# Kernel tuning notes

Measured on AMD Instinct MI355X. Metric: run time of the kernel, lower is better.

Reference implementation:

```python
import jax, jax.numpy as jnp
import numpy as np

N_EMBD = 768
N_HEAD = 12
HEAD_SIZE = N_EMBD // N_HEAD  # 64
WINDOW = 64  # sliding_window_size
EPS = 1e-6


def _rmsnorm(x, g):
    xf = x.astype(jnp.float32)
    n = xf * jax.lax.rsqrt(jnp.mean(xf * xf, axis=-1, keepdims=True) + EPS)
    return n.astype(x.dtype) * g


def _gelu_tanh(x):
    c = jnp.sqrt(jnp.asarray(2.0 / jnp.pi, x.dtype))
    return 0.5 * x * (1.0 + jnp.tanh(c * (x + 0.044715 * x ** 3)))


def setup_inputs() -> dict:
    key = jax.random.key(0)
    ks = jax.random.split(key, 12)
    B, T = 8, 1024
    s = 0.02
    return {
        "x": jax.random.normal(ks[0], (B, T, N_EMBD), jnp.float32),
        "w_q": jax.random.normal(ks[1], (N_EMBD, N_HEAD, HEAD_SIZE), jnp.float32) * s,
        "w_k": jax.random.normal(ks[2], (N_EMBD, N_HEAD, HEAD_SIZE), jnp.float32) * s,
        "w_v": jax.random.normal(ks[3], (N_EMBD, N_HEAD, HEAD_SIZE), jnp.float32) * s,
        "w_proj": jax.random.normal(ks[4], (N_EMBD, N_EMBD), jnp.float32) * s,
        "b_proj": jnp.zeros((N_EMBD,), jnp.float32),
        "w_ff1": jax.random.normal(ks[5], (N_EMBD, 4 * N_EMBD), jnp.float32) * s,
        "b_ff1": jnp.zeros((4 * N_EMBD,), jnp.float32),
        "w_ff2": jax.random.normal(ks[6], (4 * N_EMBD, N_EMBD), jnp.float32) * s,
        "b_ff2": jnp.zeros((N_EMBD,), jnp.float32),
        "g1": jnp.ones((N_EMBD,), jnp.float32),
        "g2": jnp.ones((N_EMBD,), jnp.float32),
    }


def reference(x, w_q, w_k, w_v, w_proj, b_proj, w_ff1, b_ff1, w_ff2, b_ff2, g1, g2):
    B, T, C = x.shape
    # ---- multi-head sliding-window causal attention (eval: dropout = identity) ----
    h = _rmsnorm(x, g1)
    q = jnp.einsum("btc,chd->bhtd", h, w_q)
    k = jnp.einsum("btc,chd->bhtd", h, w_k)
    v = jnp.einsum("btc,chd->bhtd", h, w_v)
    scores = jnp.einsum("bhtd,bhsd->bhts", q, k) / jnp.sqrt(jnp.asarray(HEAD_SIZE, x.dtype))
    pos = jnp.arange(T)
    diff = pos[:, None] - pos[None, :]  # q_pos - k_pos
    mask = (diff < 0) | (diff >= WINDOW)  # causal + sliding window of 64
    scores = jnp.where(mask[None, None], jnp.asarray(-jnp.inf, scores.dtype), scores)
    attn = jax.nn.softmax(scores, axis=-1)
    out = jnp.einsum("bhts,bhsd->bhtd", attn, v)
    out = out.transpose(0, 2, 1, 3).reshape(B, T, C)  # concat heads
    x = x + out @ w_proj + b_proj
    # ---- feedforward ----
    h2 = _rmsnorm(x, g2)
    ff = _gelu_tanh(h2 @ w_ff1 + b_ff1) @ w_ff2 + b_ff2
    x = x + ff
    aux = jnp.asarray(0.0, jnp.float32)
    return (x, aux)
```

## Files before the change

### kernel.cpp

```cpp
#include <hip/hip_runtime.h>
#include <cstdint>

#define DEVI __device__ __forceinline__

typedef __bf16 bf16x8 __attribute__((ext_vector_type(8)));
typedef float  f32x4  __attribute__((ext_vector_type(4)));

template<int V> struct IC { static constexpr int v = V; };

DEVI unsigned short f2b(float f){
  unsigned u = __builtin_bit_cast(unsigned, f);
  unsigned r = u + 0x7FFF + ((u >> 16) & 1);
  return (unsigned short)(r >> 16);
}
DEVI float b2f(unsigned short s){
  unsigned u = ((unsigned)s) << 16;
  return __builtin_bit_cast(float, u);
}
DEVI float gelu_f(float x){
  float u = 0.7978845608028654f * (x + 0.044715f * x * x * x);
  float e = __expf(2.0f * u);
  return x * (1.0f - 1.0f / (e + 1.0f));
}
DEVI void gl_lds16(const unsigned short* g, unsigned short* l){
  __builtin_amdgcn_global_load_lds(
      (const __attribute__((address_space(1))) unsigned int*)g,
      (__attribute__((address_space(3))) unsigned int*)l, 16, 0, 0);
}

__global__ __launch_bounds__(256)
void transpose_all(const float* __restrict__ w_q, const float* __restrict__ w_k,
                   const float* __restrict__ w_v, const float* __restrict__ w_proj,
                   const float* __restrict__ w_ff1, const float* __restrict__ w_ff2,
                   unsigned short* __restrict__ WqkvT, unsigned short* __restrict__ WprojT,
                   unsigned short* __restrict__ Wff1T, unsigned short* __restrict__ Wff2T)
{
  __shared__ float tile[32][33];
  int blk = blockIdx.x;
  const float* in; unsigned short* out; int R, C, b0;
  if      (blk < 576) { in = w_q;    out = WqkvT;              R = 768;  C = 768;  b0 = 0;    }
  else if (blk < 1152){ in = w_k;    out = WqkvT + 768 * 768;  R = 768;  C = 768;  b0 = 576;  }
  else if (blk < 1728){ in = w_v;    out = WqkvT + 1536 * 768; R = 768;  C = 768;  b0 = 1152; }
  else if (blk < 2304){ in = w_proj; out = WprojT;             R = 768;  C = 768;  b0 = 1728; }
  else if (blk < 4608){ in = w_ff1;  out = Wff1T;              R = 768;  C = 3072; b0 = 2304; }
  else                { in = w_ff2;  out = Wff2T;              R = 3072; C = 768;  b0 = 4608; }
  int lb = blk - b0;
  int nbx = C >> 5;
  int bx = lb % nbx, by = lb / nbx;
  int c0 = bx << 5, r0 = by << 5;
  int tx = threadIdx.x & 31, ty = threadIdx.x >> 5;
  #pragma unroll
  for (int j = 0; j < 32; j += 8)
    tile[ty + j][tx] = in[(size_t)(r0 + ty + j) * C + c0 + tx];
  __syncthreads();
  #pragma unroll
  for (int j = 0; j < 32; j += 8)
    out[(size_t)(c0 + ty + j) * R + r0 + tx] = f2b(tile[tx][ty + j]);
}

__global__ __launch_bounds__(256)
void rmsnorm_k(const float* __restrict__ x, const float* __restrict__ g,
               unsigned short* __restrict__ out)
{
  int wid = threadIdx.x >> 6, lane = threadIdx.x & 63;
  size_t row = (size_t)blockIdx.x * 4 + wid;
  const float* xr = x + row * 768;
  float4 v[3];
  float ss = 0.0f;
  #pragma unroll
  for (int c = 0; c < 3; c++){
    v[c] = *(const float4*)&xr[lane * 4 + c * 256];
    ss += v[c].x * v[c].x + v[c].y * v[c].y + v[c].z * v[c].z + v[c].w * v[c].w;
  }
  #pragma unroll
  for (int o = 32; o >= 1; o >>= 1) ss += __shfl_xor(ss, o);
  float rs = rsqrtf(ss * (1.0f / 768.0f) + 1e-6f);
  #pragma unroll
  for (int c = 0; c < 3; c++){
    const float4 gv = *(const float4*)&g[lane * 4 + c * 256];
    ushort4 o4;
    o4.x = f2b(v[c].x * rs * gv.x);
    o4.y = f2b(v[c].y * rs * gv.y);
    o4.z = f2b(v[c].z * rs * gv.z);
    o4.w = f2b(v[c].w * rs * gv.w);
    *(ushort4*)&out[row * 768 + lane * 4 + c * 256] = o4;
  }
}

template<bool BIAS, bool GELU_, bool RES, bool OUTF32>
__global__ __launch_bounds__(256, 3)
void gemm_db(const unsigned short* __restrict__ A, const unsigned short* __restrict__ Bt,
             const float* __restrict__ bias, const float* __restrict__ res,
             void* __restrict__ outp, int M, int N, int K)
{
  constexpr int BM = 64;
  constexpr int MI = 2;
  constexpr int AL = 2;
  constexpr int BUFSZ = (BM + 128) * 64;
  __shared__ unsigned short sm[2][BUFSZ];

  int tid = threadIdx.x, wid = tid >> 6, lane = tid & 63;
  int la = lane & 15, hi = lane >> 4;
  int wm = wid >> 1, wn = wid & 1;
  int tiles_n = N >> 7;
  int bid = blockIdx.x;
  bid = (bid & 7) * (gridDim.x >> 3) + (bid >> 3);
  int m0 = (bid / tiles_n) * BM, n0 = (bid % tiles_n) << 7;
  int NT = K >> 6;

  f32x4 acc[MI][4] = {};

  const unsigned short* aSrc[AL];
  const unsigned short* bSrc[4];
  unsigned short* aDst[2][AL];
  unsigned short* bDst[2][4];
  #pragma unroll
  for (int l = 0; l < AL; l++){
    int cb = wid * (BM * 2) + l * 64;
    int idx = cb + lane;
    int row = idx >> 3, sl2 = (idx & 7) ^ (row & 7);
    aSrc[l] = A + (size_t)(m0 + row) * K + sl2 * 8;
    aDst[0][l] = &sm[0][cb * 8];
    aDst[1][l] = &sm[1][cb * 8];
  }
  #pragma unroll
  for (int l = 0; l < 4; l++){
    int cb = wid * 256 + l * 64;
    int idx = cb + lane;
    int row = idx >> 3, sl2 = (idx & 7) ^ (row & 7);
    bSrc[l] = Bt + (size_t)(n0 + row) * K + sl2 * 8;
    bDst[0][l] = &sm[0][BM * 64 + cb * 8];
    bDst[1][l] = &sm[1][BM * 64 + cb * 8];
  }

  const unsigned short* fa[2][2];
  const unsigned short* fb[2][2];
  #pragma unroll
  for (int bf = 0; bf < 2; bf++)
    #pragma unroll
    for (int kk = 0; kk < 2; kk++){
      int sw = (((kk * 4 + hi) ^ (la & 7))) * 8;
      fa[bf][kk] = &sm[bf][(wm * (BM / 2) + la) * 64 + sw];
      fb[bf][kk] = &sm[bf][BM * 64 + (wn * 64 + la) * 64 + sw];
    }

  auto stageTo = [&](auto BF){
    constexpr int bf = decltype(BF)::v;
    #pragma unroll
    for (int l = 0; l < AL; l++){ gl_lds16(aSrc[l], aDst[bf][l]); aSrc[l] += 64; }
    #pragma unroll
    for (int l = 0; l < 4; l++){ gl_lds16(bSrc[l], bDst[bf][l]); bSrc[l] += 64; }
  };

  stageTo(IC<0>{});

  auto tile_step = [&](auto BUF, int t){
    constexpr int CB = decltype(BUF)::v;
    if (t + 1 < NT){
      stageTo(IC<CB ^ 1>{});
      asm volatile("s_waitcnt vmcnt(6)" ::: "memory");
    } else {
      asm volatile("s_waitcnt vmcnt(0)" ::: "memory");
    }
    __builtin_amdgcn_s_barrier();

    bf16x8 afr[MI][2], bfr[4][2];
    #pragma unroll
    for (int mm = 0; mm < MI; mm++){
      afr[mm][0] = *(const bf16x8*)(fa[CB][0] + mm * 1024);
      afr[mm][1] = *(const bf16x8*)(fa[CB][1] + mm * 1024);
    }
    #pragma unroll
    for (int nn = 0; nn < 4; nn++){
      bfr[nn][0] = *(const bf16x8*)(fb[CB][0] + nn * 1024);
      bfr[nn][1] = *(const bf16x8*)(fb[CB][1] + nn * 1024);
    }
    __builtin_amdgcn_s_setprio(1);
    #pragma unroll
    for (int mm = 0; mm < MI; mm++)
      #pragma unroll
      for (int nn = 0; nn < 4; nn++)
        #pragma unroll
        for (int kk = 0; kk < 2; kk++)
          acc[mm][nn] = __builtin_amdgcn_mfma_f32_16x16x32_bf16(
              afr[mm][kk], bfr[nn][kk], acc[mm][nn], 0, 0, 0);
    __builtin_amdgcn_s_setprio(0);

    __builtin_amdgcn_s_barrier();
  };

  for (int t = 0; t < NT; t += 2){
    tile_step(IC<0>{}, t);
    tile_step(IC<1>{}, t + 1);
  }

  float* outF = (float*)outp;
  unsigned short* outB = (unsigned short*)outp;
  #pragma unroll
  for (int mm = 0; mm < MI; mm++){
    int rowb = m0 + wm * (BM / 2) + mm * 16 + hi * 4;
    #pragma unroll
    for (int nn = 0; nn < 4; nn++){
      int col = n0 + wn * 64 + nn * 16 + la;
      float bv = BIAS ? bias[col] : 0.0f;
      #pragma unroll
      for (int r = 0; r < 4; r++){
        float val = acc[mm][nn][r] + bv;
        if (GELU_) val = gelu_f(val);
        if (RES)   val += res[(size_t)(rowb + r) * N + col];
        size_t o = (size_t)(rowb + r) * N + col;
        if (OUTF32) outF[o] = val;
        else        outB[o] = f2b(val);
      }
    }
  }
}

__global__ __launch_bounds__(256)
void attn_k(const unsigned short* __restrict__ qkv, unsigned short* __restrict__ attn)
{
  __shared__ unsigned short Qs[64 * 72];
  __shared__ unsigned short Ks[128 * 72];
  __shared__ unsigned short Vt[64 * 136];
  __shared__ unsigned short Ps[4][16 * 136];

  int tid = threadIdx.x, wid = tid >> 6, lane = tid & 63;
  int la = lane & 15, hi = lane >> 4;
  int blk = blockIdx.x;
  blk = (blk & 7) * (gridDim.x >> 3) + (blk >> 3);
  int tile = blk & 15, hb = blk >> 4;
  int h = hb % 12, b = hb / 12;
  int t0 = tile << 6;

  const unsigned short* qbase = qkv + (size_t)(b * 1024) * 2304 + h * 64;

  #pragma unroll
  for (int r = 0; r < 2; r++){
    int idx = tid + r * 256;
    int row = idx >> 3, ch = idx & 7;
    uint4 v = *(const uint4*)(qbase + (size_t)(t0 + row) * 2304 + ch * 8);
    *(uint4*)&Qs[row * 72 + ch * 8] = v;
  }
  #pragma unroll
  for (int r = 0; r < 4; r++){
    int idx = tid + r * 256;
    int row = idx >> 3, ch = idx & 7;
    int sg = t0 - 64 + row; sg = sg < 0 ? 0 : sg;
    uint4 v = *(const uint4*)(qbase + 768 + (size_t)sg * 2304 + ch * 8);
    *(uint4*)&Ks[row * 72 + ch * 8] = v;
  }
  #pragma unroll
  for (int r = 0; r < 4; r++){
    int idx = tid + r * 256;
    int s = idx & 127, ch = idx >> 7;
    int sg = t0 - 64 + s; sg = sg < 0 ? 0 : sg;
    uint4 v = *(const uint4*)(qbase + 1536 + (size_t)sg * 2304 + ch * 8);
    unsigned short tmp[8];
    *(uint4*)tmp = v;
    #pragma unroll
    for (int j = 0; j < 8; j++)
      Vt[(ch * 8 + j) * 136 + s] = tmp[j];
  }
  __syncthreads();

  f32x4 sc[8];
  #pragma unroll
  for (int sj = 0; sj < 8; sj++) sc[sj] = (f32x4){0.f, 0.f, 0.f, 0.f};
  #pragma unroll
  for (int kk = 0; kk < 2; kk++){
    bf16x8 aq = *(const bf16x8*)&Qs[(wid * 16 + la) * 72 + kk * 32 + hi * 8];
    #pragma unroll
    for (int sj = 0; sj < 8; sj++){
      bf16x8 bk = *(const bf16x8*)&Ks[(sj * 16 + la) * 72 + kk * 32 + hi * 8];
      sc[sj] = __builtin_amdgcn_mfma_f32_16x16x32_bf16(aq, bk, sc[sj], 0, 0, 0);
    }
  }

  float inv[4];
  #pragma unroll
  for (int r2 = 0; r2 < 4; r2++){
    int row = wid * 16 + hi * 4 + r2;
    float mx = -1e30f;
    #pragma unroll
    for (int sj = 0; sj < 8; sj++){
      int sl = sj * 16 + la;
      bool valid = (sl >= row + 1) && (sl <= row + 64) && (t0 - 64 + sl >= 0);
      float sv = valid ? sc[sj][r2] * 0.125f : -1e30f;
      sc[sj][r2] = sv;
      mx = fmaxf(mx, sv);
    }
    #pragma unroll
    for (int o = 8; o >= 1; o >>= 1) mx = fmaxf(mx, __shfl_xor(mx, o));
    float sum = 0.0f;
    #pragma unroll
    for (int sj = 0; sj < 8; sj++){
      float p = __expf(sc[sj][r2] - mx);
      sc[sj][r2] = p;
      sum += p;
    }
    #pragma unroll
    for (int o = 8; o >= 1; o >>= 1) sum += __shfl_xor(sum, o);
    inv[r2] = 1.0f / sum;
  }

  unsigned short* myP = Ps[wid];
  #pragma unroll
  for (int sj = 0; sj < 8; sj++)
    #pragma unroll
    for (int r2 = 0; r2 < 4; r2++)
      myP[(hi * 4 + r2) * 136 + sj * 16 + la] = f2b(sc[sj][r2]);

  __syncthreads();

  f32x4 oacc[4];
  #pragma unroll
  for (int nj = 0; nj < 4; nj++) oacc[nj] = (f32x4){0.f, 0.f, 0.f, 0.f};
  #pragma unroll
  for (int ks = 0; ks < 4; ks++){
    bf16x8 ap = *(const bf16x8*)&myP[la * 136 + ks * 32 + hi * 8];
    #pragma unroll
    for (int nj = 0; nj < 4; nj++){
      bf16x8 bv = *(const bf16x8*)&Vt[(nj * 16 + la) * 136 + ks * 32 + hi * 8];
      oacc[nj] = __builtin_amdgcn_mfma_f32_16x16x32_bf16(ap, bv, oacc[nj], 0, 0, 0);
    }
  }

  unsigned short* obase = attn + (size_t)(b * 1024 + t0) * 768 + h * 64;
  #pragma unroll
  for (int nj = 0; nj < 4; nj++)
    #pragma unroll
    for (int r2 = 0; r2 < 4; r2++){
      int row = wid * 16 + hi * 4 + r2;
      obase[(size_t)row * 768 + nj * 16 + la] = f2b(oacc[nj][r2] * inv[r2]);
    }
}

__global__ void aux_k(float* p){ if (threadIdx.x == 0) p[0] = 0.0f; }

extern "C" void kernel_launch(void* const* d_in, const int* in_sizes, int n_in,
                              void* d_out, int out_size, void* d_ws, size_t ws_size,
                              hipStream_t stream)
{
  const float* x      = (const float*)d_in[0];
  const float* w_q    = (const float*)d_in[1];
  const float* w_k    = (const float*)d_in[2];
  const float* w_v    = (const float*)d_in[3];
  const float* w_proj = (const float*)d_in[4];
  const float* b_proj = (const float*)d_in[5];
  const float* w_ff1  = (const float*)d_in[6];
  const float* b_ff1  = (const float*)d_in[7];
  const float* w_ff2  = (const float*)d_in[8];
  const float* b_ff2  = (const float*)d_in[9];
  const float* g1     = (const float*)d_in[10];
  const float* g2     = (const float*)d_in[11];
  float* out = (float*)d_out;

  char* ws = (char*)d_ws;
  size_t off = 0;
  auto alloc = [&](size_t bytes){ size_t r = off; off += (bytes + 255) & ~(size_t)255; return r; };
  const size_t BT = 8 * 1024;

  unsigned short* h     = (unsigned short*)(ws + alloc(BT * 768 * 2));
  unsigned short* qkv   = (unsigned short*)(ws + alloc(BT * 3072 * 2));
  float*          x2    = (float*)         (ws + alloc(BT * 768 * 4));
  unsigned short* h2    = (unsigned short*)(ws + alloc(BT * 768 * 2));
  unsigned short* WqkvT = (unsigned short*)(ws + alloc(2304 * 768 * 2));
  unsigned short* WprojT= (unsigned short*)(ws + alloc(768 * 768 * 2));
  unsigned short* Wff1T = (unsigned short*)(ws + alloc(3072 * 768 * 2));
  unsigned short* Wff2T = (unsigned short*)(ws + alloc(768 * 3072 * 2));
  unsigned short* attn  = h;
  unsigned short* ffa   = qkv;

  transpose_all<<<6912, 256, 0, stream>>>(w_q, w_k, w_v, w_proj, w_ff1, w_ff2,
                                          WqkvT, WprojT, Wff1T, Wff2T);

  rmsnorm_k<<<2048, 256, 0, stream>>>(x, g1, h);

  gemm_db<false,false,false,false><<<2304, 256, 0, stream>>>(h, WqkvT, nullptr, nullptr, qkv, 8192, 2304, 768);

  attn_k<<<8 * 12 * 16, 256, 0, stream>>>(qkv, attn);

  gemm_db<true,false,true,true><<<768, 256, 0, stream>>>(attn, WprojT, b_proj, x, x2, 8192, 768, 768);

  rmsnorm_k<<<2048, 256, 0, stream>>>(x2, g2, h2);

  gemm_db<true,true,false,false><<<3072, 256, 0, stream>>>(h2, Wff1T, b_ff1, nullptr, ffa, 8192, 3072, 768);

  gemm_db<true,false,true,true><<<768, 256, 0, stream>>>(ffa, Wff2T, b_ff2, x2, out, 8192, 768, 3072);

  aux_k<<<1, 64, 0, stream>>>(out + 6291456);
}
```

Measured before the change: 212.4 us.

## Make GEMM blocks persistent over several output tiles with cross-tile prefetch

The GEMM kernel now processes TPB consecutive output tiles per block. On the last K step it prefetches the first K slice of the next tile, so loading the next tile overlaps the current tile's final compute and epilogue. The QKV and FF1 GEMMs launch 768 blocks (3 or 4 tiles each) instead of one block per tile, which removes the per-block prologue and tail. In exchange, each block runs longer, parallelism and load balance are coarser, and the swizzled tile grouping changes, which can alter L2 reuse.

New measurement: 208.8 us. No clear change (-1.7%).

```diff
diff --git a/kernel.cpp b/kernel.cpp
--- a/kernel.cpp
+++ b/kernel.cpp
@@ -87,7 +87,7 @@
   }
 }
 
-template<bool BIAS, bool GELU_, bool RES, bool OUTF32>
+template<int TPB, bool BIAS, bool GELU_, bool RES, bool OUTF32>
 __global__ __launch_bounds__(256, 3)
 void gemm_db(const unsigned short* __restrict__ A, const unsigned short* __restrict__ Bt,
              const float* __restrict__ bias, const float* __restrict__ res,
@@ -105,21 +105,17 @@
   int tiles_n = N >> 7;
   int bid = blockIdx.x;
   bid = (bid & 7) * (gridDim.x >> 3) + (bid >> 3);
-  int m0 = (bid / tiles_n) * BM, n0 = (bid % tiles_n) << 7;
+  int g0 = bid * TPB;
   int NT = K >> 6;
 
-  f32x4 acc[MI][4] = {};
-
-  const unsigned short* aSrc[AL];
-  const unsigned short* bSrc[4];
-  unsigned short* aDst[2][AL];
-  unsigned short* bDst[2][4];
+  size_t constA[AL]; unsigned short* aDst[2][AL];
+  size_t constB[4];  unsigned short* bDst[2][4];
   #pragma unroll
   for (int l = 0; l < AL; l++){
     int cb = wid * (BM * 2) + l * 64;
     int idx = cb + lane;
     int row = idx >> 3, sl2 = (idx & 7) ^ (row & 7);
-    aSrc[l] = A + (size_t)(m0 + row) * K + sl2 * 8;
+    constA[l] = (size_t)row * K + sl2 * 8;
     aDst[0][l] = &sm[0][cb * 8];
     aDst[1][l] = &sm[1][cb * 8];
   }
@@ -128,7 +124,7 @@
     int cb = wid * 256 + l * 64;
     int idx = cb + lane;
     int row = idx >> 3, sl2 = (idx & 7) ^ (row & 7);
-    bSrc[l] = Bt + (size_t)(n0 + row) * K + sl2 * 8;
+    constB[l] = (size_t)row * K + sl2 * 8;
     bDst[0][l] = &sm[0][BM * 64 + cb * 8];
     bDst[1][l] = &sm[1][BM * 64 + cb * 8];
   }
@@ -144,6 +140,15 @@
       fb[bf][kk] = &sm[bf][BM * 64 + (wn * 64 + la) * 64 + sw];
     }
 
+  const unsigned short* aSrc[AL];
+  const unsigned short* bSrc[4];
+  auto setSrc = [&](int g){
+    int m0 = (g / tiles_n) * BM, n0 = (g % tiles_n) << 7;
+    #pragma unroll
+    for (int l = 0; l < AL; l++) aSrc[l] = A  + (size_t)m0 * K + constA[l];
+    #pragma unroll
+    for (int l = 0; l < 4;  l++) bSrc[l] = Bt + (size_t)n0 * K + constB[l];
+  };
   auto stageTo = [&](auto BF){
     constexpr int bf = decltype(BF)::v;
     #pragma unroll
@@ -152,65 +157,75 @@
     for (int l = 0; l < 4; l++){ gl_lds16(bSrc[l], bDst[bf][l]); bSrc[l] += 64; }
   };
 
+  setSrc(g0);
   stageTo(IC<0>{});
-
-  auto tile_step = [&](auto BUF, int t){
-    constexpr int CB = decltype(BUF)::v;
-    if (t + 1 < NT){
-      stageTo(IC<CB ^ 1>{});
-      asm volatile("s_waitcnt vmcnt(6)" ::: "memory");
-    } else {
-      asm volatile("s_waitcnt vmcnt(0)" ::: "memory");
-    }
-    __builtin_amdgcn_s_barrier();
-
-    bf16x8 afr[MI][2], bfr[4][2];
-    #pragma unroll
-    for (int mm = 0; mm < MI; mm++){
-      afr[mm][0] = *(const bf16x8*)(fa[CB][0] + mm * 1024);
-      afr[mm][1] = *(const bf16x8*)(fa[CB][1] + mm * 1024);
-    }
-    #pragma unroll
-    for (int nn = 0; nn < 4; nn++){
-      bfr[nn][0] = *(const bf16x8*)(fb[CB][0] + nn * 1024);
-      bfr[nn][1] = *(const bf16x8*)(fb[CB][1] + nn * 1024);
-    }
-    __builtin_amdgcn_s_setprio(1);
-    #pragma unroll
-    for (int mm = 0; mm < MI; mm++)
-      #pragma unroll
-      for (int nn = 0; nn < 4; nn++)
-        #pragma unroll
-        for (int kk = 0; kk < 2; kk++)
-          acc[mm][nn] = __builtin_amdgcn_mfma_f32_16x16x32_bf16(
-              afr[mm][kk], bfr[nn][kk], acc[mm][nn], 0, 0, 0);
-    __builtin_amdgcn_s_setprio(0);
-
-    __builtin_amdgcn_s_barrier();
-  };
-
-  for (int t = 0; t < NT; t += 2){
-    tile_step(IC<0>{}, t);
-    tile_step(IC<1>{}, t + 1);
-  }
 
   float* outF = (float*)outp;
   unsigned short* outB = (unsigned short*)outp;
-  #pragma unroll
-  for (int mm = 0; mm < MI; mm++){
-    int rowb = m0 + wm * (BM / 2) + mm * 16 + hi * 4;
-    #pragma unroll
-    for (int nn = 0; nn < 4; nn++){
-      int col = n0 + wn * 64 + nn * 16 + la;
-      float bv = BIAS ? bias[col] : 0.0f;
+
+  for (int ot = 0; ot < TPB; ot++){
+    int g = g0 + ot;
+    int m0 = (g / tiles_n) * BM, n0 = (g % tiles_n) << 7;
+
+    f32x4 acc[MI][4] = {};
+
+    auto tile_step = [&](auto BUF, int t){
+      constexpr int CB = decltype(BUF)::v;
+      if (t + 1 < NT || ot + 1 < TPB){
+        if (t + 1 == NT) setSrc(g + 1);
+        stageTo(IC<CB ^ 1>{});
+        asm volatile("s_waitcnt vmcnt(6)" ::: "memory");
+      } else {
+        asm volatile("s_waitcnt vmcnt(0)" ::: "memory");
+      }
+      __builtin_amdgcn_s_barrier();
+
+      bf16x8 afr[MI][2], bfr[4][2];
       #pragma unroll
-      for (int r = 0; r < 4; r++){
-        float val = acc[mm][nn][r] + bv;
-        if (GELU_) val = gelu_f(val);
-        if (RES)   val += res[(size_t)(rowb + r) * N + col];
-        size_t o = (size_t)(rowb + r) * N + col;
-        if (OUTF32) outF[o] = val;
-        else        outB[o] = f2b(val);
+      for (int mm = 0; mm < MI; mm++){
+        afr[mm][0] = *(const bf16x8*)(fa[CB][0] + mm * 1024);
+        afr[mm][1] = *(const bf16x8*)(fa[CB][1] + mm * 1024);
+      }
+      #pragma unroll
+      for (int nn = 0; nn < 4; nn++){
+        bfr[nn][0] = *(const bf16x8*)(fb[CB][0] + nn * 1024);
+        bfr[nn][1] = *(const bf16x8*)(fb[CB][1] + nn * 1024);
+      }
+      __builtin_amdgcn_s_setprio(1);
+      #pragma unroll
+      for (int mm = 0; mm < MI; mm++)
+        #pragma unroll
+        for (int nn = 0; nn < 4; nn++)
+          #pragma unroll
+          for (int kk = 0; kk < 2; kk++)
+            acc[mm][nn] = __builtin_amdgcn_mfma_f32_16x16x32_bf16(
+                afr[mm][kk], bfr[nn][kk], acc[mm][nn], 0, 0, 0);
+      __builtin_amdgcn_s_setprio(0);
+
+      __builtin_amdgcn_s_barrier();
+    };
+
+    for (int t = 0; t < NT; t += 2){
+      tile_step(IC<0>{}, t);
+      tile_step(IC<1>{}, t + 1);
+    }
+
+    #pragma unroll
+    for (int mm = 0; mm < MI; mm++){
+      int rowb = m0 + wm * (BM / 2) + mm * 16 + hi * 4;
+      #pragma unroll
+      for (int nn = 0; nn < 4; nn++){
+        int col = n0 + wn * 64 + nn * 16 + la;
+        float bv = BIAS ? bias[col] : 0.0f;
+        #pragma unroll
+        for (int r = 0; r < 4; r++){
+          float val = acc[mm][nn][r] + bv;
+          if (GELU_) val = gelu_f(val);
+          if (RES)   val += res[(size_t)(rowb + r) * N + col];
+          size_t o = (size_t)(rowb + r) * N + col;
+          if (OUTF32) outF[o] = val;
+          else        outB[o] = f2b(val);
+        }
       }
     }
   }
@@ -376,17 +391,17 @@
 
   rmsnorm_k<<<2048, 256, 0, stream>>>(x, g1, h);
 
-  gemm_db<false,false,false,false><<<2304, 256, 0, stream>>>(h, WqkvT, nullptr, nullptr, qkv, 8192, 2304, 768);
+  gemm_db<3,false,false,false,false><<<768, 256, 0, stream>>>(h, WqkvT, nullptr, nullptr, qkv, 8192, 2304, 768);
 
   attn_k<<<8 * 12 * 16, 256, 0, stream>>>(qkv, attn);
 
-  gemm_db<true,false,true,true><<<768, 256, 0, stream>>>(attn, WprojT, b_proj, x, x2, 8192, 768, 768);
+  gemm_db<1,true,false,true,true><<<768, 256, 0, stream>>>(attn, WprojT, b_proj, x, x2, 8192, 768, 768);
 
   rmsnorm_k<<<2048, 256, 0, stream>>>(x2, g2, h2);
 
-  gemm_db<true,true,false,false><<<3072, 256, 0, stream>>>(h2, Wff1T, b_ff1, nullptr, ffa, 8192, 3072, 768);
-
-  gemm_db<true,false,true,true><<<768, 256, 0, stream>>>(ffa, Wff2T, b_ff2, x2, out, 8192, 768, 3072);
+  gemm_db<4,true,true,false,false><<<768, 256, 0, stream>>>(h2, Wff1T, b_ff1, nullptr, ffa, 8192, 3072, 768);
+
+  gemm_db<1,true,false,true,true><<<768, 256, 0, stream>>>(ffa, Wff2T, b_ff2, x2, out, 8192, 768, 3072);
 
   aux_k<<<1, 64, 0, stream>>>(out + 6291456);
 }
```
